# Optimization experiments

Measured on AMD Instinct MI355X. Metric: run time of the kernel, lower is better.

Reference implementation:

```python
import jax, jax.numpy as jnp
import numpy as np

EMBED = 512
HEADS = 8
HD = EMBED // HEADS  # 64
NCLS = 1
WSIZE = 32
DIL = 2
WIN_LEN = 2 * WSIZE + 1  # 65


def setup_inputs() -> dict:
    key = jax.random.key(0)
    ks = jax.random.split(key, 5)
    B, S = 2, NCLS + 2048
    return {
        "x": jax.random.normal(ks[0], (B, S, EMBED), dtype=jnp.float32),
        "qkv_w": jax.random.normal(ks[1], (3 * EMBED, EMBED), dtype=jnp.float32) * 0.02,
        "qkv_b": jax.random.normal(ks[2], (3 * EMBED,), dtype=jnp.float32) * 0.02,
        "out_w": jax.random.normal(ks[3], (EMBED, EMBED), dtype=jnp.float32) * 0.02,
        "out_b": jax.random.normal(ks[4], (EMBED,), dtype=jnp.float32) * 0.02,
    }


def reference(x, qkv_w, qkv_b, out_w, out_b):
    B, S, E = x.shape
    P = S - NCLS  # patch_len
    scale = HD ** -0.5

    qkv = (x @ qkv_w.T + qkv_b).reshape(B, S, 3, HEADS, HD)
    qkv = qkv.transpose(2, 0, 3, 1, 4)  # (3, B, H, S, d)
    q, k, v = qkv[0], qkv[1], qkv[2]

    q_cls, k_cls, v_cls = q[:, :, :NCLS], k[:, :, :NCLS], v[:, :, :NCLS]
    q_p, k_p, v_p = q[:, :, NCLS:], k[:, :, NCLS:], v[:, :, NCLS:]

    # CLS queries: full attention over all S keys
    s_cls = jnp.einsum('bhqd,bhkd->bhqk', q_cls, k) * scale
    cls_out = jnp.einsum('bhqk,bhkd->bhqd', jax.nn.softmax(s_cls, axis=-1), v)

    # Patch queries: CLS keys + dilated local window
    pad = WSIZE * DIL
    kp = jnp.pad(k_p, ((0, 0), (0, 0), (pad, pad), (0, 0)))
    vp = jnp.pad(v_p, ((0, 0), (0, 0), (pad, pad), (0, 0)))
    idx = jnp.arange(P)[:, None] + jnp.arange(WIN_LEN)[None, :] * DIL  # (P, WL)
    kw = kp[:, :, idx]  # (B, H, P, WL, d)
    vw = vp[:, :, idx]

    sw = jnp.einsum('bhpd,bhpwd->bhpw', q_p, kw) * scale
    pos = jnp.arange(P)[:, None] + (jnp.arange(WIN_LEN) - WSIZE)[None, :] * DIL
    in_bounds = (pos >= 0) & (pos < P)  # (P, WL)
    sw = jnp.where(in_bounds[None, None], sw, -jnp.inf)
    sc = jnp.einsum('bhpd,bhcd->bhpc', q_p, k_cls) * scale

    attn = jax.nn.softmax(jnp.concatenate([sc, sw], axis=-1), axis=-1)
    a_c, a_w = attn[..., :NCLS], attn[..., NCLS:]
    patch_out = (jnp.einsum('bhpc,bhcd->bhpd', a_c, v_cls)
                 + jnp.einsum('bhpw,bhpwd->bhpd', a_w, vw))

    out = jnp.concatenate([cls_out, patch_out], axis=2)  # (B, H, S, d)
    out = out.transpose(0, 2, 1, 3).reshape(B, S, E)
    return out @ out_w.T + out_b
```

## Files before the change

### kernel.cpp

```cpp
#include <hip/hip_runtime.h>
#include <math.h>

#define S_LEN 2049
#define P_LEN 2048
#define EMB 512
#define NH 8
#define HD 64
#define SCALE 0.125f

typedef _Float16 f16x8 __attribute__((ext_vector_type(8)));
typedef float f32x4 __attribute__((ext_vector_type(4)));
typedef unsigned short u16x8 __attribute__((ext_vector_type(8)));

__device__ inline unsigned short f2h(float f) {
  _Float16 h = (_Float16)f;
  return __builtin_bit_cast(unsigned short, h);
}
__device__ inline float h2f(unsigned short u) {
  return (float)__builtin_bit_cast(_Float16, u);
}

__device__ inline float wave_sum64(float v) {
#pragma unroll
  for (int off = 32; off > 0; off >>= 1) v += __shfl_xor(v, off, 64);
  return v;
}

__device__ inline void gld16(const unsigned* g, unsigned* l) {
  __builtin_amdgcn_global_load_lds(
      (const __attribute__((address_space(1))) unsigned*)g,
      (__attribute__((address_space(3))) unsigned*)l, 16, 0, 0);
}

__global__ __launch_bounds__(256) void cvt3_f16(
    const float* __restrict__ s0, unsigned short* __restrict__ d0, int n0,
    const float* __restrict__ s1, unsigned short* __restrict__ d1, int n1,
    const float* __restrict__ s2, unsigned short* __restrict__ d2, int n2) {
  int idx = (blockIdx.x * 256 + threadIdx.x) * 8;
  const float* s;
  unsigned short* d;
  int off;
  if (idx < n0) {
    s = s0; d = d0; off = idx;
  } else if (idx < n0 + n1) {
    s = s1; d = d1; off = idx - n0;
  } else if (idx < n0 + n1 + n2) {
    s = s2; d = d2; off = idx - n0 - n1;
  } else {
    return;
  }
  float4 f0 = *(const float4*)(s + off);
  float4 f1 = *(const float4*)(s + off + 4);
  float ff[8] = {f0.x, f0.y, f0.z, f0.w, f1.x, f1.y, f1.z, f1.w};
  u16x8 vh;
#pragma unroll
  for (int e = 0; e < 8; e++) vh[e] = f2h(ff[e]);
  *(u16x8*)(d + off) = vh;
}

template <int BM, int BN, bool F16OUT>
__global__ __launch_bounds__(256) void gemm_f16(
    const unsigned short* __restrict__ A, const unsigned short* __restrict__ B,
    const float* __restrict__ bias, void* __restrict__ Cv, int M, int N,
    int KP) {
  constexpr int BK = 64;
  __shared__ __align__(16) unsigned short As[BM * BK];
  __shared__ __align__(16) unsigned short Bs[BN * BK];
  const int t = threadIdx.x;
  const int lane = t & 63, wv = t >> 6;
  const int m0 = blockIdx.x * BM, n0 = blockIdx.y * BN;
  constexpr int WM = BM / 2, WN = BN / 2;
  constexpr int RM = WM / 16, RN = WN / 16;
  const int wm = wv & 1, wn = wv >> 1;
  const int lm = lane & 15, lq = lane >> 4;

  f32x4 acc[RM][RN];
#pragma unroll
  for (int i = 0; i < RM; i++)
#pragma unroll
    for (int j = 0; j < RN; j++) acc[i][j] = (f32x4){0.f, 0.f, 0.f, 0.f};

  const int lr = lane >> 3;
  const int lc = (lane & 7) ^ lr;

  const unsigned* aptr[BM / 32];
#pragma unroll
  for (int p = 0; p < BM / 32; p++) {
    int ra = wv * (BM / 4) + p * 8 + lr;
    int gr = m0 + ra;
    gr = gr < M ? gr : M - 1;
    aptr[p] = (const unsigned*)(A + (size_t)gr * KP + lc * 8);
  }
  const unsigned* bptr[BN / 32];
#pragma unroll
  for (int p = 0; p < BN / 32; p++) {
    int rb = wv * (BN / 4) + p * 8 + lr;
    bptr[p] = (const unsigned*)(B + (size_t)(n0 + rb) * KP + lc * 8);
  }

  for (int kt = 0; kt < KP; kt += BK) {
    __syncthreads();
#pragma unroll
    for (int p = 0; p < BM / 32; p++)
      gld16(aptr[p] + (kt >> 1), (unsigned*)&As[(wv * (BM / 4) + p * 8) * BK]);
#pragma unroll
    for (int p = 0; p < BN / 32; p++)
      gld16(bptr[p] + (kt >> 1), (unsigned*)&Bs[(wv * (BN / 4) + p * 8) * BK]);
    __syncthreads();

    f16x8 fa[2][RM], fb[2][RN];
#pragma unroll
    for (int kk = 0; kk < 2; kk++) {
      int ch = ((kk * 4 + lq) ^ (lm & 7)) * 8;
#pragma unroll
      for (int mi = 0; mi < RM; mi++) {
        int ra = wm * WM + mi * 16 + lm;
        fa[kk][mi] = *(const f16x8*)&As[ra * BK + ch];
      }
#pragma unroll
      for (int ni = 0; ni < RN; ni++) {
        int rb = wn * WN + ni * 16 + lm;
        fb[kk][ni] = *(const f16x8*)&Bs[rb * BK + ch];
      }
    }
#pragma unroll
    for (int kk = 0; kk < 2; kk++)
#pragma unroll
      for (int mi = 0; mi < RM; mi++)
#pragma unroll
        for (int ni = 0; ni < RN; ni++)
          acc[mi][ni] = __builtin_amdgcn_mfma_f32_16x16x32_f16(
              fa[kk][mi], fb[kk][ni], acc[mi][ni], 0, 0, 0);
  }

#pragma unroll
  for (int ni = 0; ni < RN; ni++) {
    int n = n0 + wn * WN + ni * 16 + lm;
    float bv = bias[n];
#pragma unroll
    for (int mi = 0; mi < RM; mi++)
#pragma unroll
      for (int r = 0; r < 4; r++) {
        int m = m0 + wm * WM + mi * 16 + lq * 4 + r;
        if (m < M) {
          float val = acc[mi][ni][r] + bv;
          if constexpr (F16OUT)
            ((unsigned short*)Cv)[(size_t)m * N + n] = f2h(val);
          else
            ((float*)Cv)[(size_t)m * N + n] = val;
        }
      }
  }
}

__global__ __launch_bounds__(256) void patch_attn3(
    const unsigned short* __restrict__ qkv16, unsigned short* __restrict__ Aatt,
    const float* __restrict__ Pm, const float* __restrict__ Pl,
    const float* __restrict__ Po) {
  constexpr int LDK = 72;
  constexpr int LDT = 168;
  __shared__ __align__(16) unsigned short Ks[144 * LDK];
  __shared__ __align__(16) unsigned short Vt[64 * LDT];
  __shared__ __align__(16) unsigned short Ps[64 * LDT];

  const int t = threadIdx.x;
  const int qb = blockIdx.x;
  const int h = blockIdx.y;
  const int par = blockIdx.z & 1, b = blockIdx.z >> 1;

  if (qb == 16) {
    if (par == 0 && t < 64) {
      float m = -1e30f, l = 0.f, o = 0.f;
      for (int ck = 0; ck < 32; ck++) {
        int idx = (b * NH + h) * 32 + ck;
        float mc = Pm[idx];
        float lc = Pl[idx];
        float oc = Po[(size_t)idx * 64 + t];
        float mn = fmaxf(m, mc);
        float e0 = __expf(m - mn);
        float e1 = __expf(mc - mn);
        l = l * e0 + lc * e1;
        o = o * e0 + oc * e1;
        m = mn;
      }
      Aatt[(size_t)b * S_LEN * 512 + h * HD + t] = f2h(o / l);
    }
    return;
  }

  const int lane = t & 63, wv = t >> 6;
  const int lm = lane & 15, lq = lane >> 4;
  const unsigned short* base = qkv16 + (size_t)b * S_LEN * 1536;
  const int qc0 = qb * 64;

  {
    uint4 z = {0, 0, 0, 0};
    if (t < 135) {
      int row = 129 + t / 9, q = t % 9;
      *(uint4*)&Ks[row * LDK + q * 8] = z;
    }
    {
      int row = t >> 2, q = t & 3;
      *(uint4*)&Vt[row * LDT + 128 + q * 8] = z;
    }
    if (t < 128) {
      int row = t >> 1, q = t & 1;
      *(uint4*)&Ps[row * LDT + 144 + q * 8] = z;
    }
  }
  __syncthreads();

  {
    int rr = t >> 4;
    int cc = (t & 15) * 4;
#pragma unroll
    for (int pass = 0; pass < 8; pass++) {
      int r = pass * 16 + rr;
      int jc = qc0 - 32 + r;
      uint2 kv = {0, 0};
      if ((unsigned)jc < 1024u)
        kv = *(const uint2*)(base + (size_t)(1 + 2 * jc + par) * 1536 + 512 +
                             h * 64 + cc);
      *(uint2*)&Ks[r * LDK + cc] = kv;
    }
    if (rr == 0)
      *(uint2*)&Ks[128 * LDK + cc] = *(const uint2*)(base + 512 + h * 64 + cc);
  }
#pragma unroll
  for (int pass = 0; pass < 4; pass++) {
    int task = pass * 256 + t;
    int jp = task >> 4;
    int d0 = (task & 15) * 4;
    int jc0 = qc0 - 32 + 2 * jp;
    uint2 a = {0, 0}, c = {0, 0};
    if ((unsigned)jc0 < 1024u)
      a = *(const uint2*)(base + (size_t)(1 + 2 * jc0 + par) * 1536 + 1024 +
                          h * 64 + d0);
    if ((unsigned)(jc0 + 1) < 1024u)
      c = *(const uint2*)(base + (size_t)(1 + 2 * (jc0 + 1) + par) * 1536 +
                          1024 + h * 64 + d0);
    *(unsigned*)&Vt[(d0 + 0) * LDT + 2 * jp] = (a.x & 0xffffu) | (c.x << 16);
    *(unsigned*)&Vt[(d0 + 1) * LDT + 2 * jp] = (a.x >> 16) | (c.x & 0xffff0000u);
    *(unsigned*)&Vt[(d0 + 2) * LDT + 2 * jp] = (a.y & 0xffffu) | (c.y << 16);
    *(unsigned*)&Vt[(d0 + 3) * LDT + 2 * jp] = (a.y >> 16) | (c.y & 0xffff0000u);
  }
  if (t < 64) Vt[t * LDT + 128] = base[1024 + h * 64 + t];

  const int qi = wv * 16 + lm;
  const unsigned short* qg =
      base + (size_t)(1 + 2 * (qc0 + qi) + par) * 1536 + h * 64;
  f16x8 qf[2];
  qf[0] = *(const f16x8*)&qg[lq * 8];
  qf[1] = *(const f16x8*)&qg[32 + lq * 8];
  __syncthreads();

  f32x4 s[9];
#pragma unroll
  for (int nt = 0; nt < 9; nt++) s[nt] = (f32x4){0.f, 0.f, 0.f, 0.f};
#pragma unroll
  for (int nt = 0; nt < 9; nt++) {
#pragma unroll
    for (int kk = 0; kk < 2; kk++) {
      f16x8 kb = *(const f16x8*)&Ks[(nt * 16 + lm) * LDK + kk * 32 + lq * 8];
      s[nt] =
          __builtin_amdgcn_mfma_f32_16x16x32_f16(qf[kk], kb, s[nt], 0, 0, 0);
    }
  }

  float L[4];
#pragma unroll
  for (int r = 0; r < 4; r++) {
    int qrow = wv * 16 + lq * 4 + r;
    float sv[9];
    float mx = -1e30f;
#pragma unroll
    for (int nt = 0; nt < 9; nt++) {
      int jl = nt * 16 + lm;
      bool valid =
          (jl == 128) ||
          (jl < 128 && jl >= qrow && jl <= qrow + 64 &&
           (unsigned)(qc0 - 32 + jl) < 1024u);
      sv[nt] = valid ? s[nt][r] * SCALE : -1e30f;
      mx = fmaxf(mx, sv[nt]);
    }
#pragma unroll
    for (int off = 1; off < 16; off <<= 1)
      mx = fmaxf(mx, __shfl_xor(mx, off, 16));
    float l = 0.f;
#pragma unroll
    for (int nt = 0; nt < 9; nt++) {
      float e = __expf(sv[nt] - mx);
      l += e;
      Ps[qrow * LDT + nt * 16 + lm] = f2h(e);
    }
#pragma unroll
    for (int off = 1; off < 16; off <<= 1) l += __shfl_xor(l, off, 16);
    L[r] = l;
  }
  __syncthreads();

  f32x4 oa[4];
#pragma unroll
  for (int nt = 0; nt < 4; nt++) oa[nt] = (f32x4){0.f, 0.f, 0.f, 0.f};
#pragma unroll
  for (int kc = 0; kc < 5; kc++) {
    f16x8 pa = *(const f16x8*)&Ps[(wv * 16 + lm) * LDT + kc * 32 + lq * 8];
#pragma unroll
    for (int nt = 0; nt < 4; nt++) {
      f16x8 vb = *(const f16x8*)&Vt[(nt * 16 + lm) * LDT + kc * 32 + lq * 8];
      oa[nt] = __builtin_amdgcn_mfma_f32_16x16x32_f16(pa, vb, oa[nt], 0, 0, 0);
    }
  }

#pragma unroll
  for (int r = 0; r < 4; r++) {
    float inv = 1.f / L[r];
    int qrow = wv * 16 + lq * 4 + r;
    int pp = 2 * (qc0 + qrow) + par;
    unsigned short* ab = Aatt + ((size_t)b * S_LEN + 1 + pp) * 512 + h * 64;
#pragma unroll
    for (int nt = 0; nt < 4; nt++) ab[nt * 16 + lm] = f2h(oa[nt][r] * inv);
  }
}

__global__ __launch_bounds__(256) void cls_part_k(
    const unsigned short* __restrict__ qkv16, float* __restrict__ Pm,
    float* __restrict__ Pl, float* __restrict__ Po) {
  const int lane = threadIdx.x & 63;
  const int wv = threadIdx.x >> 6;
  const int ck = blockIdx.x;
  const int h = blockIdx.y;
  const int b = blockIdx.z;
  const unsigned short* base = qkv16 + (size_t)b * S_LEN * 1536;
  float qd = h2f(base[h * 64 + lane]) * SCALE;

  int c0 = ck * 64;
  int cend = (ck == 31) ? S_LEN : c0 + 64;

  float m = -1e30f, l = 0.f, o = 0.f;
  for (int j = c0 + wv; j < cend; j += 4) {
    const unsigned short* krow = base + (size_t)j * 1536 + 512 + h * 64;
    float kv = h2f(krow[lane]);
    float vv = h2f(krow[512 + lane]);
    float s = wave_sum64(qd * kv);
    float mn = fmaxf(m, s);
    float e0 = __expf(m - mn);
    float e1 = __expf(s - mn);
    l = l * e0 + e1;
    o = o * e0 + e1 * vv;
    m = mn;
  }

  __shared__ float sm[4], sl[4], so[4][64];
  if (lane == 0) {
    sm[wv] = m;
    sl[wv] = l;
  }
  so[wv][lane] = o;
  __syncthreads();
  if (wv == 0) {
    float M = -1e30f;
#pragma unroll
    for (int i = 0; i < 4; i++) M = fmaxf(M, sm[i]);
    float L = 0.f, O = 0.f;
#pragma unroll
    for (int i = 0; i < 4; i++) {
      float c = __expf(sm[i] - M);
      L += sl[i] * c;
      O += so[i][lane] * c;
    }
    int idx = (b * NH + h) * 32 + ck;
    if (lane == 0) {
      Pm[idx] = M;
      Pl[idx] = L;
    }
    Po[(size_t)idx * 64 + lane] = O;
  }
}

extern "C" void kernel_launch(void* const* d_in, const int* in_sizes, int n_in,
                              void* d_out, int out_size, void* d_ws,
                              size_t ws_size, hipStream_t stream) {
  const float* x = (const float*)d_in[0];
  const float* qkv_w = (const float*)d_in[1];
  const float* qkv_b = (const float*)d_in[2];
  const float* out_w = (const float*)d_in[3];
  const float* out_b = (const float*)d_in[4];
  float* out = (float*)d_out;

  const int M = 2 * S_LEN;

  float* cls_pm = (float*)d_ws;
  float* cls_pl = cls_pm + 512;
  float* cls_po = cls_pl + 512;
  unsigned short* Xp = (unsigned short*)(cls_po + 32768);
  unsigned short* Wq = Xp + (size_t)M * 512;
  unsigned short* Wo = Wq + (size_t)1536 * 512;
  unsigned short* Aatt = Wo + (size_t)512 * 512;
  unsigned short* qkv16 = Aatt + (size_t)M * 512;

  const int n0 = M * EMB;
  const int n1 = 1536 * EMB;
  const int n2 = EMB * EMB;
  int cvt_blocks = ((n0 + n1 + n2) / 8 + 255) / 256;
  cvt3_f16<<<cvt_blocks, 256, 0, stream>>>(x, Xp, n0, qkv_w, Wq, n1, out_w, Wo,
                                           n2);

  dim3 gq((M + 63) / 64, 1536 / 128);
  gemm_f16<64, 128, true><<<gq, 256, 0, stream>>>(Xp, Wq, qkv_b, qkv16, M,
                                                  1536, 512);

  cls_part_k<<<dim3(32, NH, 2), 256, 0, stream>>>(qkv16, cls_pm, cls_pl,
                                                  cls_po);
  patch_attn3<<<dim3(17, NH, 4), 256, 0, stream>>>(qkv16, Aatt, cls_pm, cls_pl,
                                                   cls_po);

  dim3 go((M + 63) / 64, EMB / 64);
  gemm_f16<64, 64, false><<<go, 256, 0, stream>>>(Aatt, Wo, out_b, out, M, EMB,
                                                  512);
}
```

Baseline: 123.0 us.

## Fuse CLS-token attention into patch attention kernel using last-block atomic reduction

Removes the separate cls_part_k launch and the extra reduction block. Each patch-attention block reuses the K and V tiles it already holds in shared memory to compute a partial softmax (max, sum, weighted V) for the CLS query over its 64 keys. A per-(batch, head) atomic counter, zeroed in the conversion kernel, lets the last finishing block merge the 32 partials plus the CLS key itself and write the CLS output. This saves a kernel launch and the re-read of K/V, at the cost of extra per-block work and threadfence/atomic synchronisation.

```diff
diff --git a/kernel.cpp b/kernel.cpp
--- a/kernel.cpp
+++ b/kernel.cpp
@@ -20,12 +20,6 @@
   return (float)__builtin_bit_cast(_Float16, u);
 }
 
-__device__ inline float wave_sum64(float v) {
-#pragma unroll
-  for (int off = 32; off > 0; off >>= 1) v += __shfl_xor(v, off, 64);
-  return v;
-}
-
 __device__ inline void gld16(const unsigned* g, unsigned* l) {
   __builtin_amdgcn_global_load_lds(
       (const __attribute__((address_space(1))) unsigned*)g,
@@ -35,7 +29,9 @@
 __global__ __launch_bounds__(256) void cvt3_f16(
     const float* __restrict__ s0, unsigned short* __restrict__ d0, int n0,
     const float* __restrict__ s1, unsigned short* __restrict__ d1, int n1,
-    const float* __restrict__ s2, unsigned short* __restrict__ d2, int n2) {
+    const float* __restrict__ s2, unsigned short* __restrict__ d2, int n2,
+    unsigned* __restrict__ counters) {
+  if (blockIdx.x == 0 && threadIdx.x < 16) counters[threadIdx.x] = 0;
   int idx = (blockIdx.x * 256 + threadIdx.x) * 8;
   const float* s;
   unsigned short* d;
@@ -153,41 +149,22 @@
   }
 }
 
-__global__ __launch_bounds__(256) void patch_attn3(
+__global__ __launch_bounds__(256) void patch_attn4(
     const unsigned short* __restrict__ qkv16, unsigned short* __restrict__ Aatt,
-    const float* __restrict__ Pm, const float* __restrict__ Pl,
-    const float* __restrict__ Po) {
+    float* __restrict__ Pm, float* __restrict__ Pl, float* __restrict__ Po,
+    unsigned* __restrict__ counters) {
   constexpr int LDK = 72;
   constexpr int LDT = 168;
   __shared__ __align__(16) unsigned short Ks[144 * LDK];
   __shared__ __align__(16) unsigned short Vt[64 * LDT];
   __shared__ __align__(16) unsigned short Ps[64 * LDT];
+  __shared__ float sbuf[64], ebuf[64];
+  __shared__ int clsflag;
 
   const int t = threadIdx.x;
   const int qb = blockIdx.x;
   const int h = blockIdx.y;
   const int par = blockIdx.z & 1, b = blockIdx.z >> 1;
-
-  if (qb == 16) {
-    if (par == 0 && t < 64) {
-      float m = -1e30f, l = 0.f, o = 0.f;
-      for (int ck = 0; ck < 32; ck++) {
-        int idx = (b * NH + h) * 32 + ck;
-        float mc = Pm[idx];
-        float lc = Pl[idx];
-        float oc = Po[(size_t)idx * 64 + t];
-        float mn = fmaxf(m, mc);
-        float e0 = __expf(m - mn);
-        float e1 = __expf(mc - mn);
-        l = l * e0 + lc * e1;
-        o = o * e0 + oc * e1;
-        m = mn;
-      }
-      Aatt[(size_t)b * S_LEN * 512 + h * HD + t] = f2h(o / l);
-    }
-    return;
-  }
-
   const int lane = t & 63, wv = t >> 6;
   const int lm = lane & 15, lq = lane >> 4;
   const unsigned short* base = qkv16 + (size_t)b * S_LEN * 1536;
@@ -321,60 +298,73 @@
 #pragma unroll
     for (int nt = 0; nt < 4; nt++) ab[nt * 16 + lm] = f2h(oa[nt][r] * inv);
   }
-}
-
-__global__ __launch_bounds__(256) void cls_part_k(
-    const unsigned short* __restrict__ qkv16, float* __restrict__ Pm,
-    float* __restrict__ Pl, float* __restrict__ Po) {
-  const int lane = threadIdx.x & 63;
-  const int wv = threadIdx.x >> 6;
-  const int ck = blockIdx.x;
-  const int h = blockIdx.y;
-  const int b = blockIdx.z;
-  const unsigned short* base = qkv16 + (size_t)b * S_LEN * 1536;
-  float qd = h2f(base[h * 64 + lane]) * SCALE;
-
-  int c0 = ck * 64;
-  int cend = (ck == 31) ? S_LEN : c0 + 64;
-
-  float m = -1e30f, l = 0.f, o = 0.f;
-  for (int j = c0 + wv; j < cend; j += 4) {
-    const unsigned short* krow = base + (size_t)j * 1536 + 512 + h * 64;
-    float kv = h2f(krow[lane]);
-    float vv = h2f(krow[512 + lane]);
-    float s = wave_sum64(qd * kv);
-    float mn = fmaxf(m, s);
+
+  const int pidx = ((b * NH + h) * 2 + par) * 16 + qb;
+  {
+    int r = t >> 2, dq = t & 3;
+    float sp = 0.f;
+#pragma unroll
+    for (int j = 0; j < 16; j++)
+      sp += h2f(base[h * 64 + dq * 16 + j]) *
+            h2f(Ks[(32 + r) * LDK + dq * 16 + j]);
+    sp += __shfl_xor(sp, 1, 4);
+    sp += __shfl_xor(sp, 2, 4);
+    if (dq == 0) sbuf[r] = sp * SCALE;
+  }
+  __syncthreads();
+  if (wv == 0) {
+    float sv = sbuf[lane];
+    float mx = sv;
+#pragma unroll
+    for (int off = 32; off > 0; off >>= 1)
+      mx = fmaxf(mx, __shfl_xor(mx, off, 64));
+    float e = __expf(sv - mx);
+    ebuf[lane] = e;
+    float l = e;
+#pragma unroll
+    for (int off = 32; off > 0; off >>= 1) l += __shfl_xor(l, off, 64);
+    if (lane == 0) {
+      Pm[pidx] = mx;
+      Pl[pidx] = l;
+    }
+    float o = 0.f;
+    for (int r2 = 0; r2 < 64; r2++)
+      o += ebuf[r2] * h2f(Vt[lane * LDT + 32 + r2]);
+    Po[(size_t)pidx * 64 + lane] = o;
+  }
+  __syncthreads();
+  if (t == 0) {
+    __threadfence();
+    unsigned old = atomicAdd(&counters[b * NH + h], 1u);
+    clsflag = (old == 31);
+  }
+  __syncthreads();
+  if (clsflag && t < 64) {
+    __threadfence();
+    float m = -1e30f, l = 0.f, o = 0.f;
+    int pb = (b * NH + h) * 32;
+    for (int k = 0; k < 32; k++) {
+      float mc = Pm[pb + k];
+      float lc = Pl[pb + k];
+      float oc = Po[(size_t)(pb + k) * 64 + t];
+      float mn = fmaxf(m, mc);
+      float e0 = __expf(m - mn);
+      float e1 = __expf(mc - mn);
+      l = l * e0 + lc * e1;
+      o = o * e0 + oc * e1;
+      m = mn;
+    }
+    float p = h2f(base[h * 64 + t]) * h2f(base[512 + h * 64 + t]);
+#pragma unroll
+    for (int off = 32; off > 0; off >>= 1) p += __shfl_xor(p, off, 64);
+    float s0 = p * SCALE;
+    float vv = h2f(base[1024 + h * 64 + t]);
+    float mn = fmaxf(m, s0);
     float e0 = __expf(m - mn);
-    float e1 = __expf(s - mn);
+    float e1 = __expf(s0 - mn);
     l = l * e0 + e1;
     o = o * e0 + e1 * vv;
-    m = mn;
-  }
-
-  __shared__ float sm[4], sl[4], so[4][64];
-  if (lane == 0) {
-    sm[wv] = m;
-    sl[wv] = l;
-  }
-  so[wv][lane] = o;
-  __syncthreads();
-  if (wv == 0) {
-    float M = -1e30f;
-#pragma unroll
-    for (int i = 0; i < 4; i++) M = fmaxf(M, sm[i]);
-    float L = 0.f, O = 0.f;
-#pragma unroll
-    for (int i = 0; i < 4; i++) {
-      float c = __expf(sm[i] - M);
-      L += sl[i] * c;
-      O += so[i][lane] * c;
-    }
-    int idx = (b * NH + h) * 32 + ck;
-    if (lane == 0) {
-      Pm[idx] = M;
-      Pl[idx] = L;
-    }
-    Po[(size_t)idx * 64 + lane] = O;
+    Aatt[(size_t)b * S_LEN * 512 + h * 64 + t] = f2h(o / l);
   }
 }
 
@@ -393,7 +383,8 @@
   float* cls_pm = (float*)d_ws;
   float* cls_pl = cls_pm + 512;
   float* cls_po = cls_pl + 512;
-  unsigned short* Xp = (unsigned short*)(cls_po + 32768);
+  unsigned* counters = (unsigned*)(cls_po + 32768);
+  unsigned short* Xp = (unsigned short*)(counters + 16);
   unsigned short* Wq = Xp + (size_t)M * 512;
   unsigned short* Wo = Wq + (size_t)1536 * 512;
   unsigned short* Aatt = Wo + (size_t)512 * 512;
@@ -404,16 +395,14 @@
   const int n2 = EMB * EMB;
   int cvt_blocks = ((n0 + n1 + n2) / 8 + 255) / 256;
   cvt3_f16<<<cvt_blocks, 256, 0, stream>>>(x, Xp, n0, qkv_w, Wq, n1, out_w, Wo,
-                                           n2);
+                                           n2, counters);
 
   dim3 gq((M + 63) / 64, 1536 / 128);
   gemm_f16<64, 128, true><<<gq, 256, 0, stream>>>(Xp, Wq, qkv_b, qkv16, M,
                                                   1536, 512);
 
-  cls_part_k<<<dim3(32, NH, 2), 256, 0, stream>>>(qkv16, cls_pm, cls_pl,
-                                                  cls_po);
-  patch_attn3<<<dim3(17, NH, 4), 256, 0, stream>>>(qkv16, Aatt, cls_pm, cls_pl,
-                                                   cls_po);
+  patch_attn4<<<dim3(16, NH, 4), 256, 0, stream>>>(qkv16, Aatt, cls_pm, cls_pl,
+                                                   cls_po, counters);
 
   dim3 go((M + 63) / 64, EMB / 64);
   gemm_f16<64, 64, false><<<go, 256, 0, stream>>>(Aatt, Wo, out_b, out, M, EMB,
```

Result: slower. 135.6 us (+10.2%).
